# Kernel tuning notes

Hardware: AMD Instinct MI355X
Metric: run time of the kernel (lower is better)

Reference implementation:

```python
import jax, jax.numpy as jnp
import numpy as np

N, E, C, H = 50000, 800000, 64, 64  # nodes, edges, channels, mlp hidden


def _seg_softmax(logits, seg, num_segments):
    # per-destination-node, per-channel softmax over incoming edges (PyG softmax)
    m = jax.ops.segment_max(logits, seg, num_segments=num_segments)
    m = jnp.where(jnp.isfinite(m), m, 0.0)
    e = jnp.exp(logits - m[seg])
    s = jax.ops.segment_sum(e, seg, num_segments=num_segments)
    return e / (s[seg] + 1e-16)


def setup_inputs() -> dict:
    key = jax.random.key(0)
    ks = jax.random.split(key, 16)

    def w(k, shape, fan_in):
        lim = 1.0 / np.sqrt(fan_in)
        return jax.random.uniform(k, shape, jnp.float32, -lim, lim)

    return dict(
        x=jax.random.normal(ks[0], (N, C), jnp.float32),
        pos=jax.random.uniform(ks[1], (N, 3), jnp.float32),
        edge_index=jax.random.randint(ks[2], (2, E), 0, N),
        # lin_in (Linear with bias)
        W_in=w(ks[3], (C, C), C), b_in=jnp.zeros((C,), jnp.float32),
        # PointTransformerConv internal linears (bias=False in PyG)
        W_lin=w(ks[4], (C, C), C),
        W_src=w(ks[5], (C, C), C),
        W_dst=w(ks[6], (C, C), C),
        # pos_nn: Linear(3,64) + ReLU + Linear(64,C)
        Wp1=w(ks[7], (3, H), 3), bp1=jnp.zeros((H,), jnp.float32),
        Wp2=w(ks[8], (H, C), H), bp2=jnp.zeros((C,), jnp.float32),
        # attn_nn: Linear(C,64) + ReLU + Linear(64,C)
        Wa1=w(ks[9], (C, H), C), ba1=jnp.zeros((H,), jnp.float32),
        Wa2=w(ks[10], (H, C), H), ba2=jnp.zeros((C,), jnp.float32),
        # lin_out
        W_out=w(ks[11], (C, C), C), b_out=jnp.zeros((C,), jnp.float32),
    )


def reference(x, pos, edge_index, W_in, b_in, W_lin, W_src, W_dst,
              Wp1, bp1, Wp2, bp2, Wa1, ba1, Wa2, ba2, W_out, b_out):
    n = x.shape[0]
    src, dst = edge_index[0], edge_index[1]
    # lin_in + ReLU
    h = jax.nn.relu(x @ W_in + b_in)                      # [N,C]
    # PointTransformerConv projections
    v = h @ W_lin                                         # values [N,C]
    a_src = h @ W_src                                     # alpha_j source term
    a_dst = h @ W_dst                                     # alpha_i dest term
    # per-edge positional encoding: pos_nn(pos_i - pos_j)
    rel = pos[dst] - pos[src]                             # [E,3]
    delta = jax.nn.relu(rel @ Wp1 + bp1) @ Wp2 + bp2      # [E,C]
    # attention logits: attn_nn(alpha_i - alpha_j + delta)
    alpha = a_dst[dst] - a_src[src] + delta               # [E,C]
    alpha = jax.nn.relu(alpha @ Wa1 + ba1) @ Wa2 + ba2    # [E,C]
    alpha = _seg_softmax(alpha, dst, n)
    # weighted scatter-sum aggregation: sum_j alpha * (x_j + delta)
    out = jax.ops.segment_sum(alpha * (v[src] + delta), dst, num_segments=n)
    # lin_out + ReLU
    return jax.nn.relu(out @ W_out + b_out)
```

## Files before the change

### kernel.cpp

```cpp
#include <hip/hip_runtime.h>

typedef unsigned short u16;
typedef unsigned int   u32;
typedef unsigned long long u64;
typedef __attribute__((ext_vector_type(8))) short bf16x8;
typedef __attribute__((ext_vector_type(4))) float f32x4;

#define DEV static __device__ __forceinline__

DEV u16 f2bf(float f){ union{float f; u32 i;} v; v.f=f; u32 u=v.i;
                       return (u16)((u + 0x7FFFu + ((u>>16)&1u))>>16); }
DEV float bf2f(u16 u){ union{u32 i; float f;} v; v.i=((u32)u)<<16; return v.f; }
DEV float bfl(u32 w){ return bf2f((u16)(w & 0xffffu)); }
DEV float bfh(u32 w){ return bf2f((u16)(w >> 16)); }
DEV u32 pk2(float a, float b){ return (u32)f2bf(a) | ((u32)f2bf(b) << 16); }
DEV void ldsfence(){ asm volatile("s_waitcnt lgkmcnt(0)" ::: "memory"); }
DEV void ldsorder(){ asm volatile("" ::: "memory"); }

#define NBIAS 384
#define FB_P1 0
#define FB_P2 4
#define FB_A1 12
#define FB_A2 20
#define FB_IN 28
#define FB_LIN 36
#define FB_SRC 44
#define FB_DST 52
#define FB_OUT 60
#define NFRAG 68

#define LROW 70
#define LROWD 35

DEV bf16x8 fb_load(const u16* __restrict__ FB, int frag, int lane){
  union{ uint4 u; bf16x8 v; } w;
  w.u = *(const uint4*)(FB + ((size_t)(frag*64+lane))*8);
  return w.v;
}
DEV bf16x8 lds_read_chunk(const u32* l32, int dw){
  union{ u32 d[4]; bf16x8 v; } u;
#pragma unroll
  for(int p=0;p<4;p++) u.d[p] = l32[dw+p];
  return u.v;
}

#define PREP_BLOCKS 19
__global__ __launch_bounds__(256) void k_prep(
  const float* __restrict__ Win, const float* __restrict__ Wlin,
  const float* __restrict__ Wsrc, const float* __restrict__ Wdst,
  const float* __restrict__ Wp1, const float* __restrict__ Wp2,
  const float* __restrict__ Wa1, const float* __restrict__ Wa2,
  const float* __restrict__ Wout,
  const float* __restrict__ bin, const float* __restrict__ bp1, const float* __restrict__ bp2,
  const float* __restrict__ ba1, const float* __restrict__ ba2, const float* __restrict__ bout,
  float* __restrict__ Bf, u16* __restrict__ FB,
  const int* __restrict__ ei, int* __restrict__ deg, int E)
{
  if(blockIdx.x >= PREP_BLOCKS){
    int e = (blockIdx.x - PREP_BLOCKS)*256 + threadIdx.x;
    if(e < E) atomicAdd(&deg[ei[(size_t)E + e]], 1);
    return;
  }
  int idx = blockIdx.x*256 + threadIdx.x;
  if(idx < NBIAS){
    int which = idx >> 6, c = idx & 63;
    if(which == 3){
      float sacc = ba1[c];
      for(int k=0;k<64;k++) sacc += bp2[k]*Wa1[k*64+c];
      Bf[idx] = sacc;
    } else {
      const float* b;
      switch(which){ case 0:b=bin;break; case 1:b=bp1;break; case 2:b=bp2;break;
                     case 4:b=ba2;break; default:b=bout;break; }
      Bf[idx] = b[c];
    }
  } else if(idx < NBIAS + NFRAG*64){
    int j = idx - NBIAS;
    int frag = j >> 6, lane = j & 63;
    int t = lane & 15, q = lane >> 4;
    const float* src = nullptr; const float* fuse = nullptr;
    int K = 64, nt, s;
    if(frag < 4){ src = Wp1; K = 3; nt = frag; s = 0; }
    else if(frag < 12){ int g=frag-4;  src=Wp2;  nt=g>>1; s=g&1; }
    else if(frag < 20){ int g=frag-12; fuse=Wp2; nt=g>>1; s=g&1; }
    else if(frag < 28){ int g=frag-20; src=Wa2;  nt=g>>1; s=g&1; }
    else if(frag < 36){ int g=frag-28; src=Win;  nt=g>>1; s=g&1; }
    else if(frag < 44){ int g=frag-36; src=Wlin; nt=g>>1; s=g&1; }
    else if(frag < 52){ int g=frag-44; fuse=Wsrc; nt=g>>1; s=g&1; }
    else if(frag < 60){ int g=frag-52; fuse=Wdst; nt=g>>1; s=g&1; }
    else              { int g=frag-60; src=Wout; nt=g>>1; s=g&1; }
    u16* dst = FB + ((size_t)(frag*64+lane))*8;
    if(fuse){
      int col = nt*16 + t;
#pragma unroll
      for(int jj=0;jj<8;jj++){
        int k = s*32 + q*8 + jj;
        const float* ar = fuse + k*64;
        float accv = 0.f;
        for(int m=0;m<64;m++) accv += ar[m] * Wa1[m*64+col];
        dst[jj] = f2bf(accv);
      }
    } else {
#pragma unroll
      for(int jj=0;jj<8;jj++){
        int k = s*32 + q*8 + jj;
        dst[jj] = (k<K) ? f2bf(src[k*64 + nt*16 + t]) : (u16)0;
      }
    }
  }
}

__global__ __launch_bounds__(256) void k_scanA(const int* __restrict__ deg,
    int* __restrict__ row_start, int* __restrict__ bsum, int N){
  __shared__ int b[256];
  int tid = threadIdx.x, i = blockIdx.x*256 + tid;
  int v = (i<N) ? deg[i] : 0;
  b[tid] = v; __syncthreads();
#pragma unroll
  for(int off=1; off<256; off<<=1){
    int u = (tid>=off) ? b[tid-off] : 0;
    __syncthreads(); b[tid] += u; __syncthreads();
  }
  if(i<N) row_start[i] = b[tid] - v;
  if(tid==255) bsum[blockIdx.x] = b[255];
}

__global__ __launch_bounds__(256) void k_scanBC(
  const int* __restrict__ bsum, int* __restrict__ row_start, int nb, int N)
{
  __shared__ int b[256];
  __shared__ int ex[256];
  int tid = threadIdx.x;
  int v = (tid<nb) ? bsum[tid] : 0;
  b[tid] = v; __syncthreads();
#pragma unroll
  for(int off=1; off<256; off<<=1){
    int u = (tid>=off) ? b[tid-off] : 0;
    __syncthreads(); b[tid] += u; __syncthreads();
  }
  ex[tid] = b[tid] - v;
  __syncthreads();
  int off0 = ex[blockIdx.x];
  int i = blockIdx.x*256 + tid;
  if(i<N) row_start[i] += off0;
  if(blockIdx.x==0 && tid==255) row_start[N] = b[255];
}

__global__ __launch_bounds__(256) void k_mid2(
  const int* __restrict__ ei, const int* __restrict__ row_start, int* __restrict__ cursor,
  int2* __restrict__ pair, int E, int sblocks,
  const float* __restrict__ x, const float* __restrict__ Bf, const u16* __restrict__ FB,
  u16* __restrict__ vf, u16* __restrict__ asof, u16* __restrict__ adof,
  int N, int ntiles, int nodeblocks,
  float* __restrict__ Z, int zcount4, int zblocks)
{
  __shared__ u16 sc16[4][16*LROW];
  int bid = blockIdx.x;

  if(bid < sblocks){
    int e = bid*256 + threadIdx.x;
    if(e < E){
      int d = ei[(size_t)E + e];
      int p = atomicAdd(&cursor[d], 1);
      int2 pr; pr.x = ei[e]; pr.y = d;
      pair[row_start[d] + p] = pr;
    }
    return;
  }
  if(bid >= sblocks + nodeblocks){
    int zb = bid - sblocks - nodeblocks;
    float4* Z4 = (float4*)Z;
    float4 z = {0.f,0.f,0.f,0.f};
    for(int i = zb*256 + threadIdx.x; i < zcount4; i += zblocks*256) Z4[i] = z;
    return;
  }

  int lane = threadIdx.x & 63, warp = threadIdx.x >> 6;
  int t = lane & 15, q = lane >> 4;
  int tile = (bid - sblocks)*4 + warp;
  if(tile >= ntiles) return;
  u16* lb = sc16[warp]; u32* lb32 = (u32*)lb;
  int r0 = tile*16;
  int row = r0 + t; if(row >= N) row = N-1;

  const float4* x4 = (const float4*)(x + (size_t)row*64);
  bf16x8 xa[2];
#pragma unroll
  for(int s=0;s<2;s++){
    float4 u0 = x4[s*8 + q*2], u1 = x4[s*8 + q*2 + 1];
    xa[s][0]=(short)f2bf(u0.x); xa[s][1]=(short)f2bf(u0.y);
    xa[s][2]=(short)f2bf(u0.z); xa[s][3]=(short)f2bf(u0.w);
    xa[s][4]=(short)f2bf(u1.x); xa[s][5]=(short)f2bf(u1.y);
    xa[s][6]=(short)f2bf(u1.z); xa[s][7]=(short)f2bf(u1.w);
  }
  f32x4 zero = {0.f,0.f,0.f,0.f};
  f32x4 acc[4];
#pragma unroll
  for(int nt=0;nt<4;nt++){
    acc[nt] = __builtin_amdgcn_mfma_f32_16x16x32_bf16(xa[0], fb_load(FB, FB_IN+nt*2+0, lane), zero, 0,0,0);
    acc[nt] = __builtin_amdgcn_mfma_f32_16x16x32_bf16(xa[1], fb_load(FB, FB_IN+nt*2+1, lane), acc[nt], 0,0,0);
  }
#pragma unroll
  for(int nt=0;nt<4;nt++)
#pragma unroll
    for(int r=0;r<4;r++)
      lb[(q*4+r)*LROW + nt*16 + t] = f2bf(fmaxf(acc[nt][r] + Bf[nt*16+t], 0.f));
  ldsfence();
  bf16x8 h0 = lds_read_chunk(lb32, t*LROWD + q*4);
  bf16x8 h1 = lds_read_chunk(lb32, t*LROWD + 16 + q*4);

  const int fb0[3] = {FB_LIN, FB_SRC, FB_DST};
  u16* Os[3] = {vf, asof, adof};
#pragma unroll
  for(int mtx=0; mtx<3; mtx++){
    f32x4 av[4];
#pragma unroll
    for(int nt=0;nt<4;nt++){
      av[nt] = __builtin_amdgcn_mfma_f32_16x16x32_bf16(h0, fb_load(FB, fb0[mtx]+nt*2+0, lane), zero, 0,0,0);
      av[nt] = __builtin_amdgcn_mfma_f32_16x16x32_bf16(h1, fb_load(FB, fb0[mtx]+nt*2+1, lane), av[nt], 0,0,0);
    }
    u16* O = Os[mtx];
#pragma unroll
    for(int r=0;r<4;r++){
      int rr = r0 + q*4 + r;
      if(rr < N){
        uint2 o;
        o.x = (u32)f2bf(av[0][r]) | ((u32)f2bf(av[1][r]) << 16);
        o.y = (u32)f2bf(av[2][r]) | ((u32)f2bf(av[3][r]) << 16);
        *(uint2*)(O + (size_t)rr*64 + t*4) = o;
      }
    }
  }
}

DEV void flushseg(int d, float* numP, float* SP, const int* __restrict__ row_start,
                  float* __restrict__ num, float* __restrict__ S,
                  int lo, int hi, int q, int t){
  if(d < 0) return;
#pragma unroll
  for(int nt=0;nt<4;nt++){
    numP[nt] += __shfl_xor(numP[nt], 16, 64);
    numP[nt] += __shfl_xor(numP[nt], 32, 64);
    SP[nt]   += __shfl_xor(SP[nt],   16, 64);
    SP[nt]   += __shfl_xor(SP[nt],   32, 64);
  }
  bool partial = (row_start[d] < lo) || (row_start[d+1] > hi);
  if(q==0){
#pragma unroll
    for(int nt=0;nt<4;nt++){
      size_t off = (size_t)d*64 + nt*16 + t;
      if(partial){ atomicAdd(&num[off], numP[nt]); atomicAdd(&S[off], SP[nt]); }
      else       { num[off] = numP[nt]; S[off] = SP[nt]; }
    }
  }
#pragma unroll
  for(int nt=0;nt<4;nt++){ numP[nt]=0.f; SP[nt]=0.f; }
}

DEV void agg_tile(int tbase, int hi_w, int lo_w, int did,
                  const float wv[4][4], const float pd[4][4],
                  int& cur_d, float* numP, float* SP,
                  const int* __restrict__ row_start,
                  float* __restrict__ num, float* __restrict__ S, int q, int t){
  int m = 0;
  while(m < 16){
    int d0 = __shfl(did, m, 64);
    u32 same = (u32)(__ballot(did == d0) & 0xFFFFull);
    u32 rest = ~(same >> m);
    int len = __ffs(rest) - 1;
    int m1 = m + len;
    if(d0 != cur_d){
      flushseg(cur_d, numP, SP, row_start, num, S, lo_w, hi_w, q, t);
      cur_d = d0;
    }
#pragma unroll
    for(int r=0;r<4;r++){
      int mm = q*4 + r;
      bool use = (mm >= m) && (mm < m1) && ((tbase+mm) < hi_w);
      if(use){
#pragma unroll
        for(int nt=0;nt<4;nt++){
          numP[nt] += wv[nt][r] * pd[r][nt];
          SP[nt]   += wv[nt][r];
        }
      }
    }
    m = m1;
  }
}

__global__ __launch_bounds__(256,2) void k_edge_p9(
  const int* __restrict__ row_start, const int2* __restrict__ pair,
  const float* __restrict__ pos, const float* __restrict__ Bf, const u16* __restrict__ FB,
  const u16* __restrict__ vf, const u16* __restrict__ asof, const u16* __restrict__ adof,
  float* __restrict__ S, float* __restrict__ num, int E, int nsuper, int spw)
{
  __shared__ u16 sc16[4][2*32*LROW];
  int lane = threadIdx.x & 63, warp = threadIdx.x >> 6;
  int t = lane & 15, q = lane >> 4;
  int wid = blockIdx.x*4 + warp;
  int s0 = wid*spw, s1 = s0 + spw;
  if(s0 >= nsuper) return;
  if(s1 > nsuper) s1 = nsuper;
  int lo = s0*32, hi = s1*32; if(hi > E) hi = E;
  u16* lb = sc16[warp];             u32* lb32 = (u32*)lb;
  u16* lu = sc16[warp] + 32*LROW;   u32* lu32 = (u32*)lu;

  float bp1f[4], bp2f[4], baf[4], ba2f[4];
#pragma unroll
  for(int nt=0;nt<4;nt++){
    bp1f[nt]=Bf[ 64+nt*16+t]; bp2f[nt]=Bf[128+nt*16+t];
    baf[nt] =Bf[192+nt*16+t]; ba2f[nt]=Bf[256+nt*16+t];
  }
  const uint2* ad2 = (const uint2*)adof;
  const uint2* as2 = (const uint2*)asof;
  const uint2* v2  = (const uint2*)vf;
  f32x4 zero = {0.f,0.f,0.f,0.f};
  float numP[4] = {0,0,0,0}, SP[4] = {0,0,0,0};
  int cur_d = -1;

  int2 spA, spB;
  bf16x8 a1A, a1B;
  {
    int ecA = lo + t;      if(ecA >= hi) ecA = hi-1;
    int ecB = lo + 16 + t; if(ecB >= hi) ecB = hi-1;
    spA = pair[ecA]; spB = pair[ecB];
#pragma unroll
    for(int j=0;j<8;j++){ a1A[j]=0; a1B[j]=0; }
    if(q==0){
      a1A[0] = (short)f2bf(pos[(size_t)spA.y*3+0] - pos[(size_t)spA.x*3+0]);
      a1A[1] = (short)f2bf(pos[(size_t)spA.y*3+1] - pos[(size_t)spA.x*3+1]);
      a1A[2] = (short)f2bf(pos[(size_t)spA.y*3+2] - pos[(size_t)spA.x*3+2]);
      a1B[0] = (short)f2bf(pos[(size_t)spB.y*3+0] - pos[(size_t)spB.x*3+0]);
      a1B[1] = (short)f2bf(pos[(size_t)spB.y*3+1] - pos[(size_t)spB.x*3+1]);
      a1B[2] = (short)f2bf(pos[(size_t)spB.y*3+2] - pos[(size_t)spB.x*3+2]);
    }
  }

  for(int tb = lo; tb < hi; tb += 32){
    bool hasB = (tb+16) < hi;
    int didA = spA.y, didB = spB.y;

    int2 nspA, nspB;
    {
      int eA = tb + 32 + t; if(eA >= hi) eA = hi-1;
      int eB = tb + 48 + t; if(eB >= hi) eB = hi-1;
      nspA = pair[eA]; nspB = pair[eB];
    }
    uint2 adwA[4], aswA[4];
#pragma unroll
    for(int r=0;r<4;r++){
      int e = tb + q*4 + r; if(e >= hi) e = hi-1;
      int2 p = pair[e];
      adwA[r] = ad2[(size_t)p.y*16 + t];
      aswA[r] = as2[(size_t)p.x*16 + t];
    }
    uint2 adwB[4], aswB[4];
#pragma unroll
    for(int r=0;r<4;r++){
      int e = tb + 16 + q*4 + r; if(e >= hi) e = hi-1;
      int2 p = pair[e];
      adwB[r] = ad2[(size_t)p.y*16 + t];
      aswB[r] = as2[(size_t)p.x*16 + t];
    }
    uint2 vrawA[4], vrawB[4];
#pragma unroll
    for(int r=0;r<4;r++){
      int e = tb + q*4 + r; if(e >= hi) e = hi-1;
      vrawA[r] = v2[(size_t)pair[e].x*16 + t];
    }
#pragma unroll
    for(int r=0;r<4;r++){
      int e = tb + 16 + q*4 + r; if(e >= hi) e = hi-1;
      vrawB[r] = v2[(size_t)pair[e].x*16 + t];
    }

    f32x4 accA[4], accB[4];
#pragma unroll
    for(int nt=0;nt<4;nt++){
      bf16x8 wp = fb_load(FB, FB_P1+nt, lane);
      accA[nt] = __builtin_amdgcn_mfma_f32_16x16x32_bf16(a1A, wp, zero, 0,0,0);
      accB[nt] = __builtin_amdgcn_mfma_f32_16x16x32_bf16(a1B, wp, zero, 0,0,0);
    }

#pragma unroll
    for(int nt=0;nt<4;nt++)
#pragma unroll
      for(int r=0;r<4;r++){
        lb[(     q*4+r)*LROW + nt*16 + t] = f2bf(fmaxf(accA[nt][r] + bp1f[nt], 0.f));
        lb[(16 + q*4+r)*LROW + nt*16 + t] = f2bf(fmaxf(accB[nt][r] + bp1f[nt], 0.f));
      }
    ldsorder();

    bf16x8 atA0 = lds_read_chunk(lb32, (t   )*LROWD + q*4);
    bf16x8 atA1 = lds_read_chunk(lb32, (t   )*LROWD + 16 + q*4);
    bf16x8 atB0 = lds_read_chunk(lb32, (t+16)*LROWD + q*4);
    bf16x8 atB1 = lds_read_chunk(lb32, (t+16)*LROWD + 16 + q*4);

    bf16x8 na1A, na1B;
#pragma unroll
    for(int j=0;j<8;j++){ na1A[j]=0; na1B[j]=0; }
    if(q==0){
      na1A[0] = (short)f2bf(pos[(size_t)nspA.y*3+0] - pos[(size_t)nspA.x*3+0]);
      na1A[1] = (short)f2bf(pos[(size_t)nspA.y*3+1] - pos[(size_t)nspA.x*3+1]);
      na1A[2] = (short)f2bf(pos[(size_t)nspA.y*3+2] - pos[(size_t)nspA.x*3+2]);
      na1B[0] = (short)f2bf(pos[(size_t)nspB.y*3+0] - pos[(size_t)nspB.x*3+0]);
      na1B[1] = (short)f2bf(pos[(size_t)nspB.y*3+1] - pos[(size_t)nspB.x*3+1]);
      na1B[2] = (short)f2bf(pos[(size_t)nspB.y*3+2] - pos[(size_t)nspB.x*3+2]);
    }

    u32 dpA[4][2], dpB[4][2];
#pragma unroll
    for(int nt=0;nt<4;nt++){
      bf16x8 w0 = fb_load(FB, FB_P2+nt*2+0, lane);
      bf16x8 w1 = fb_load(FB, FB_P2+nt*2+1, lane);
      f32x4 a = __builtin_amdgcn_mfma_f32_16x16x32_bf16(atA0, w0, zero, 0,0,0);
      a = __builtin_amdgcn_mfma_f32_16x16x32_bf16(atA1, w1, a, 0,0,0);
      f32x4 b = __builtin_amdgcn_mfma_f32_16x16x32_bf16(atB0, w0, zero, 0,0,0);
      b = __builtin_amdgcn_mfma_f32_16x16x32_bf16(atB1, w1, b, 0,0,0);
      dpA[nt][0] = pk2(a[0]+bp2f[nt], a[1]+bp2f[nt]);
      dpA[nt][1] = pk2(a[2]+bp2f[nt], a[3]+bp2f[nt]);
      dpB[nt][0] = pk2(b[0]+bp2f[nt], b[1]+bp2f[nt]);
      dpB[nt][1] = pk2(b[2]+bp2f[nt], b[3]+bp2f[nt]);
    }

#pragma unroll
    for(int nt=0;nt<4;nt++){
      bf16x8 w0 = fb_load(FB, FB_A1+nt*2+0, lane);
      bf16x8 w1 = fb_load(FB, FB_A1+nt*2+1, lane);
      f32x4 a = __builtin_amdgcn_mfma_f32_16x16x32_bf16(atA0, w0, zero, 0,0,0);
      a = __builtin_amdgcn_mfma_f32_16x16x32_bf16(atA1, w1, a, 0,0,0);
#pragma unroll
      for(int r=0;r<4;r++){
        u32 dw = (nt&2)? adwA[r].y : adwA[r].x;
        u32 sw = (nt&2)? aswA[r].y : aswA[r].x;
        float c = ((nt&1)? bfh(dw) : bfl(dw)) - ((nt&1)? bfh(sw) : bfl(sw));
        lu[(q*4+r)*LROW + nt*16 + t] = f2bf(fmaxf(a[r] + c + baf[nt], 0.f));
      }
    }
#pragma unroll
    for(int nt=0;nt<4;nt++){
      bf16x8 w0 = fb_load(FB, FB_A1+nt*2+0, lane);
      bf16x8 w1 = fb_load(FB, FB_A1+nt*2+1, lane);
      f32x4 b = __builtin_amdgcn_mfma_f32_16x16x32_bf16(atB0, w0, zero, 0,0,0);
      b = __builtin_amdgcn_mfma_f32_16x16x32_bf16(atB1, w1, b, 0,0,0);
#pragma unroll
      for(int r=0;r<4;r++){
        u32 dw = (nt&2)? adwB[r].y : adwB[r].x;
        u32 sw = (nt&2)? aswB[r].y : aswB[r].x;
        float c = ((nt&1)? bfh(dw) : bfl(dw)) - ((nt&1)? bfh(sw) : bfl(sw));
        lu[(16 + q*4+r)*LROW + nt*16 + t] = f2bf(fmaxf(b[r] + c + baf[nt], 0.f));
      }
    }
    ldsorder();

    bf16x8 auA0 = lds_read_chunk(lu32, (t   )*LROWD + q*4);
    bf16x8 auA1 = lds_read_chunk(lu32, (t   )*LROWD + 16 + q*4);
    bf16x8 auB0 = lds_read_chunk(lu32, (t+16)*LROWD + q*4);
    bf16x8 auB1 = lds_read_chunk(lu32, (t+16)*LROWD + 16 + q*4);

    float wv[4][4], pd[4][4];
#pragma unroll
    for(int nt=0;nt<4;nt++){
      bf16x8 w0 = fb_load(FB, FB_A2+nt*2+0, lane);
      bf16x8 w1 = fb_load(FB, FB_A2+nt*2+1, lane);
      f32x4 a = __builtin_amdgcn_mfma_f32_16x16x32_bf16(auA0, w0, zero, 0,0,0);
      a = __builtin_amdgcn_mfma_f32_16x16x32_bf16(auA1, w1, a, 0,0,0);
#pragma unroll
      for(int r=0;r<4;r++)
        wv[nt][r] = ((tb + q*4 + r) < hi) ? __expf(fminf(a[r] + ba2f[nt], 80.f)) : 0.f;
    }
#pragma unroll
    for(int r=0;r<4;r++){
      float va[4] = { bfl(vrawA[r].x), bfh(vrawA[r].x), bfl(vrawA[r].y), bfh(vrawA[r].y) };
#pragma unroll
      for(int nt=0;nt<4;nt++){
        u32 dw = dpA[nt][r>>1];
        pd[r][nt] = va[nt] + ((r&1)? bfh(dw) : bfl(dw));
      }
    }
    agg_tile(tb, hi, lo, didA, wv, pd, cur_d, numP, SP, row_start, num, S, q, t);

    if(hasB){
#pragma unroll
      for(int nt=0;nt<4;nt++){
        bf16x8 w0 = fb_load(FB, FB_A2+nt*2+0, lane);
        bf16x8 w1 = fb_load(FB, FB_A2+nt*2+1, lane);
        f32x4 b = __builtin_amdgcn_mfma_f32_16x16x32_bf16(auB0, w0, zero, 0,0,0);
        b = __builtin_amdgcn_mfma_f32_16x16x32_bf16(auB1, w1, b, 0,0,0);
#pragma unroll
        for(int r=0;r<4;r++)
          wv[nt][r] = ((tb + 16 + q*4 + r) < hi) ? __expf(fminf(b[r] + ba2f[nt], 80.f)) : 0.f;
      }
#pragma unroll
      for(int r=0;r<4;r++){
        float vb[4] = { bfl(vrawB[r].x), bfh(vrawB[r].x), bfl(vrawB[r].y), bfh(vrawB[r].y) };
#pragma unroll
        for(int nt=0;nt<4;nt++){
          u32 dw = dpB[nt][r>>1];
          pd[r][nt] = vb[nt] + ((r&1)? bfh(dw) : bfl(dw));
        }
      }
      agg_tile(tb+16, hi, lo, didB, wv, pd, cur_d, numP, SP, row_start, num, S, q, t);
    }

    spA = nspA; spB = nspB; a1A = na1A; a1B = na1B;
  }
  flushseg(cur_d, numP, SP, row_start, num, S, lo, hi, q, t);
}

__global__ __launch_bounds__(256) void k_out_m(
  const float* __restrict__ num, const float* __restrict__ S,
  const float* __restrict__ Bf, const u16* __restrict__ FB,
  float* __restrict__ out, int N, int ntiles)
{
  int lane = threadIdx.x & 63, warp = threadIdx.x >> 6;
  int t = lane & 15, q = lane >> 4;
  int tile = blockIdx.x*4 + warp;
  if(tile >= ntiles) return;
  int r0 = tile*16;
  int row = r0 + t; if(row >= N) row = N-1;
  const float4* n4 = (const float4*)(num + (size_t)row*64);
  const float4* s4 = (const float4*)(S   + (size_t)row*64);
  bf16x8 af[2];
#pragma unroll
  for(int s=0;s<2;s++){
    float4 n0 = n4[s*8 + q*2], n1 = n4[s*8 + q*2 + 1];
    float4 s0 = s4[s*8 + q*2], s1 = s4[s*8 + q*2 + 1];
    af[s][0]=(short)f2bf(n0.x/(s0.x+1e-16f)); af[s][1]=(short)f2bf(n0.y/(s0.y+1e-16f));
    af[s][2]=(short)f2bf(n0.z/(s0.z+1e-16f)); af[s][3]=(short)f2bf(n0.w/(s0.w+1e-16f));
    af[s][4]=(short)f2bf(n1.x/(s1.x+1e-16f)); af[s][5]=(short)f2bf(n1.y/(s1.y+1e-16f));
    af[s][6]=(short)f2bf(n1.z/(s1.z+1e-16f)); af[s][7]=(short)f2bf(n1.w/(s1.w+1e-16f));
  }
  f32x4 zero = {0.f,0.f,0.f,0.f};
#pragma unroll
  for(int nt=0;nt<4;nt++){
    f32x4 a = __builtin_amdgcn_mfma_f32_16x16x32_bf16(af[0], fb_load(FB, FB_OUT+nt*2+0, lane), zero, 0,0,0);
    a = __builtin_amdgcn_mfma_f32_16x16x32_bf16(af[1], fb_load(FB, FB_OUT+nt*2+1, lane), a, 0,0,0);
    float b = Bf[320 + nt*16 + t];
#pragma unroll
    for(int r=0;r<4;r++){
      int rr = r0 + q*4 + r;
      if(rr < N) out[(size_t)rr*64 + nt*16 + t] = fmaxf(a[r] + b, 0.f);
    }
  }
}

extern "C" void kernel_launch(void* const* d_in, const int* in_sizes, int n_in,
                              void* d_out, int out_size, void* d_ws, size_t ws_size,
                              hipStream_t stream){
  const float* x   =(const float*)d_in[0];
  const float* pos =(const float*)d_in[1];
  const int*   ei  =(const int*)d_in[2];
  const float* Win =(const float*)d_in[3];  const float* bin=(const float*)d_in[4];
  const float* Wlin=(const float*)d_in[5];  const float* Wsrc=(const float*)d_in[6];
  const float* Wdst=(const float*)d_in[7];
  const float* Wp1 =(const float*)d_in[8];  const float* bp1=(const float*)d_in[9];
  const float* Wp2 =(const float*)d_in[10]; const float* bp2=(const float*)d_in[11];
  const float* Wa1 =(const float*)d_in[12]; const float* ba1=(const float*)d_in[13];
  const float* Wa2 =(const float*)d_in[14]; const float* ba2=(const float*)d_in[15];
  const float* Wout=(const float*)d_in[16]; const float* bout=(const float*)d_in[17];
  int N = in_sizes[0]/64;
  int E = in_sizes[2]/2;

  float* Bf    = (float*)d_ws;
  u16*   FB    = (u16*)(Bf + NBIAS);
  u16*   vfb   = FB + (size_t)NFRAG*64*8;
  u16*   asb   = vfb + (size_t)N*64;
  u16*   adb   = asb + (size_t)N*64;
  float* S     = (float*)(adb + (size_t)N*64);
  float* num   = S    + (size_t)N*64;
  int* deg       = (int*)(num + (size_t)N*64);
  int* cursor    = deg + N;
  int* row_start = cursor + N;
  int* bsum      = row_start + (N+1);
  int* bsoff     = bsum + 256;
  int2* pair     = (int2*)(bsoff + 256);

  int ntiles = (N+15)/16;
  int nsuper = (E+31)/32;
  int total_waves = 2048;
  int spw = (nsuper + total_waves - 1) / total_waves;
  int nwaves = (nsuper + spw - 1) / spw;
  int eblocks = (nwaves + 3) / 4;
  int nscb = (N+255)/256;
  int hblocks = (E+255)/256;
  int nodeblocks = (ntiles+3)/4;
  int sblocks = (E+255)/256;
  int zblocks = 512;
  int zcount4 = N*32;

  hipMemsetAsync(deg, 0, (size_t)2*N*sizeof(int), stream);
  k_prep<<<dim3(PREP_BLOCKS + hblocks), dim3(256), 0, stream>>>(
      Win,Wlin,Wsrc,Wdst,Wp1,Wp2,Wa1,Wa2,Wout,
      bin,bp1,bp2,ba1,ba2,bout, Bf, FB, ei, deg, E);
  k_scanA<<<dim3(nscb), dim3(256), 0, stream>>>(deg, row_start, bsum, N);
  k_scanBC<<<dim3(nscb), dim3(256), 0, stream>>>(bsum, row_start, nscb, N);
  k_mid2<<<dim3(sblocks + nodeblocks + zblocks), dim3(256), 0, stream>>>(
      ei, row_start, cursor, pair, E, sblocks,
      x, Bf, FB, vfb, asb, adb, N, ntiles, nodeblocks,
      S, zcount4, zblocks);
  k_edge_p9<<<dim3(eblocks), dim3(256), 0, stream>>>(row_start, pair, pos, Bf, FB,
                                                     vfb, asb, adb, S, num, E, nsuper, spw);
  k_out_m<<<dim3((ntiles+3)/4), dim3(256), 0, stream>>>(num, S, Bf, FB, (float*)d_out, N, ntiles);
}
```

Baseline: 331.5 us.

## Process three 16-edge sub-tiles per edge-kernel iteration and defer value gathers

The edge kernel now handles 48 edges per loop iteration (three 16-row MFMA sub-tiles A/B/C) instead of 32. The per-warp LDS scratch and the super-tile size grow to match. The value-vector gathers move later, after the attention first-layer MFMAs, so their latency can overlap with compute. The aim is more independent gathers and MFMAs in flight per iteration, at the cost of more registers and LDS, which may cut occupancy under launch_bounds(256,2) or cause spills.

```diff
diff --git a/kernel.cpp b/kernel.cpp
--- a/kernel.cpp
+++ b/kernel.cpp
@@ -289,22 +289,22 @@
   }
 }
 
-__global__ __launch_bounds__(256,2) void k_edge_p9(
+__global__ __launch_bounds__(256,2) void k_edge_p10(
   const int* __restrict__ row_start, const int2* __restrict__ pair,
   const float* __restrict__ pos, const float* __restrict__ Bf, const u16* __restrict__ FB,
   const u16* __restrict__ vf, const u16* __restrict__ asof, const u16* __restrict__ adof,
   float* __restrict__ S, float* __restrict__ num, int E, int nsuper, int spw)
 {
-  __shared__ u16 sc16[4][2*32*LROW];
+  __shared__ u16 sc16[4][2*48*LROW];
   int lane = threadIdx.x & 63, warp = threadIdx.x >> 6;
   int t = lane & 15, q = lane >> 4;
   int wid = blockIdx.x*4 + warp;
   int s0 = wid*spw, s1 = s0 + spw;
   if(s0 >= nsuper) return;
   if(s1 > nsuper) s1 = nsuper;
-  int lo = s0*32, hi = s1*32; if(hi > E) hi = E;
+  int lo = s0*48, hi = s1*48; if(hi > E) hi = E;
   u16* lb = sc16[warp];             u32* lb32 = (u32*)lb;
-  u16* lu = sc16[warp] + 32*LROW;   u32* lu32 = (u32*)lu;
+  u16* lu = sc16[warp] + 48*LROW;   u32* lu32 = (u32*)lu;
 
   float bp1f[4], bp2f[4], baf[4], ba2f[4];
 #pragma unroll
@@ -319,14 +319,15 @@
   float numP[4] = {0,0,0,0}, SP[4] = {0,0,0,0};
   int cur_d = -1;
 
-  int2 spA, spB;
-  bf16x8 a1A, a1B;
+  int2 spA, spB, spC;
+  bf16x8 a1A, a1B, a1C;
   {
     int ecA = lo + t;      if(ecA >= hi) ecA = hi-1;
     int ecB = lo + 16 + t; if(ecB >= hi) ecB = hi-1;
-    spA = pair[ecA]; spB = pair[ecB];
-#pragma unroll
-    for(int j=0;j<8;j++){ a1A[j]=0; a1B[j]=0; }
+    int ecC = lo + 32 + t; if(ecC >= hi) ecC = hi-1;
+    spA = pair[ecA]; spB = pair[ecB]; spC = pair[ecC];
+#pragma unroll
+    for(int j=0;j<8;j++){ a1A[j]=0; a1B[j]=0; a1C[j]=0; }
     if(q==0){
       a1A[0] = (short)f2bf(pos[(size_t)spA.y*3+0] - pos[(size_t)spA.x*3+0]);
       a1A[1] = (short)f2bf(pos[(size_t)spA.y*3+1] - pos[(size_t)spA.x*3+1]);
@@ -334,18 +335,22 @@
       a1B[0] = (short)f2bf(pos[(size_t)spB.y*3+0] - pos[(size_t)spB.x*3+0]);
       a1B[1] = (short)f2bf(pos[(size_t)spB.y*3+1] - pos[(size_t)spB.x*3+1]);
       a1B[2] = (short)f2bf(pos[(size_t)spB.y*3+2] - pos[(size_t)spB.x*3+2]);
-    }
-  }
-
-  for(int tb = lo; tb < hi; tb += 32){
-    bool hasB = (tb+16) < hi;
-    int didA = spA.y, didB = spB.y;
-
-    int2 nspA, nspB;
+      a1C[0] = (short)f2bf(pos[(size_t)spC.y*3+0] - pos[(size_t)spC.x*3+0]);
+      a1C[1] = (short)f2bf(pos[(size_t)spC.y*3+1] - pos[(size_t)spC.x*3+1]);
+      a1C[2] = (short)f2bf(pos[(size_t)spC.y*3+2] - pos[(size_t)spC.x*3+2]);
+    }
+  }
+
+  for(int tb = lo; tb < hi; tb += 48){
+    bool hasB = (tb+16) < hi, hasC = (tb+32) < hi;
+    int didA = spA.y, didB = spB.y, didC = spC.y;
+
+    int2 nspA, nspB, nspC;
     {
-      int eA = tb + 32 + t; if(eA >= hi) eA = hi-1;
-      int eB = tb + 48 + t; if(eB >= hi) eB = hi-1;
-      nspA = pair[eA]; nspB = pair[eB];
+      int eA = tb + 48 + t; if(eA >= hi) eA = hi-1;
+      int eB = tb + 64 + t; if(eB >= hi) eB = hi-1;
+      int eC = tb + 80 + t; if(eC >= hi) eC = hi-1;
+      nspA = pair[eA]; nspB = pair[eB]; nspC = pair[eC];
     }
     uint2 adwA[4], aswA[4];
 #pragma unroll
@@ -363,24 +368,14 @@
       adwB[r] = ad2[(size_t)p.y*16 + t];
       aswB[r] = as2[(size_t)p.x*16 + t];
     }
-    uint2 vrawA[4], vrawB[4];
-#pragma unroll
-    for(int r=0;r<4;r++){
-      int e = tb + q*4 + r; if(e >= hi) e = hi-1;
-      vrawA[r] = v2[(size_t)pair[e].x*16 + t];
-    }
-#pragma unroll
-    for(int r=0;r<4;r++){
-      int e = tb + 16 + q*4 + r; if(e >= hi) e = hi-1;
-      vrawB[r] = v2[(size_t)pair[e].x*16 + t];
-    }
-
-    f32x4 accA[4], accB[4];
+
+    f32x4 accA[4], accB[4], accC[4];
 #pragma unroll
     for(int nt=0;nt<4;nt++){
       bf16x8 wp = fb_load(FB, FB_P1+nt, lane);
       accA[nt] = __builtin_amdgcn_mfma_f32_16x16x32_bf16(a1A, wp, zero, 0,0,0);
       accB[nt] = __builtin_amdgcn_mfma_f32_16x16x32_bf16(a1B, wp, zero, 0,0,0);
+      accC[nt] = __builtin_amdgcn_mfma_f32_16x16x32_bf16(a1C, wp, zero, 0,0,0);
     }
 
 #pragma unroll
@@ -389,6 +384,7 @@
       for(int r=0;r<4;r++){
         lb[(     q*4+r)*LROW + nt*16 + t] = f2bf(fmaxf(accA[nt][r] + bp1f[nt], 0.f));
         lb[(16 + q*4+r)*LROW + nt*16 + t] = f2bf(fmaxf(accB[nt][r] + bp1f[nt], 0.f));
+        lb[(32 + q*4+r)*LROW + nt*16 + t] = f2bf(fmaxf(accC[nt][r] + bp1f[nt], 0.f));
       }
     ldsorder();
 
@@ -396,10 +392,12 @@
     bf16x8 atA1 = lds_read_chunk(lb32, (t   )*LROWD + 16 + q*4);
     bf16x8 atB0 = lds_read_chunk(lb32, (t+16)*LROWD + q*4);
     bf16x8 atB1 = lds_read_chunk(lb32, (t+16)*LROWD + 16 + q*4);
-
-    bf16x8 na1A, na1B;
-#pragma unroll
-    for(int j=0;j<8;j++){ na1A[j]=0; na1B[j]=0; }
+    bf16x8 atC0 = lds_read_chunk(lb32, (t+32)*LROWD + q*4);
+    bf16x8 atC1 = lds_read_chunk(lb32, (t+32)*LROWD + 16 + q*4);
+
+    bf16x8 na1A, na1B, na1C;
+#pragma unroll
+    for(int j=0;j<8;j++){ na1A[j]=0; na1B[j]=0; na1C[j]=0; }
     if(q==0){
       na1A[0] = (short)f2bf(pos[(size_t)nspA.y*3+0] - pos[(size_t)nspA.x*3+0]);
       na1A[1] = (short)f2bf(pos[(size_t)nspA.y*3+1] - pos[(size_t)nspA.x*3+1]);
@@ -407,9 +405,12 @@
       na1B[0] = (short)f2bf(pos[(size_t)nspB.y*3+0] - pos[(size_t)nspB.x*3+0]);
       na1B[1] = (short)f2bf(pos[(size_t)nspB.y*3+1] - pos[(size_t)nspB.x*3+1]);
       na1B[2] = (short)f2bf(pos[(size_t)nspB.y*3+2] - pos[(size_t)nspB.x*3+2]);
-    }
-
-    u32 dpA[4][2], dpB[4][2];
+      na1C[0] = (short)f2bf(pos[(size_t)nspC.y*3+0] - pos[(size_t)nspC.x*3+0]);
+      na1C[1] = (short)f2bf(pos[(size_t)nspC.y*3+1] - pos[(size_t)nspC.x*3+1]);
+      na1C[2] = (short)f2bf(pos[(size_t)nspC.y*3+2] - pos[(size_t)nspC.x*3+2]);
+    }
+
+    u32 dpA[4][2], dpB[4][2], dpC[4][2];
 #pragma unroll
     for(int nt=0;nt<4;nt++){
       bf16x8 w0 = fb_load(FB, FB_P2+nt*2+0, lane);
@@ -418,18 +419,20 @@
       a = __builtin_amdgcn_mfma_f32_16x16x32_bf16(atA1, w1, a, 0,0,0);
       f32x4 b = __builtin_amdgcn_mfma_f32_16x16x32_bf16(atB0, w0, zero, 0,0,0);
       b = __builtin_amdgcn_mfma_f32_16x16x32_bf16(atB1, w1, b, 0,0,0);
+      f32x4 c = __builtin_amdgcn_mfma_f32_16x16x32_bf16(atC0, w0, zero, 0,0,0);
+      c = __builtin_amdgcn_mfma_f32_16x16x32_bf16(atC1, w1, c, 0,0,0);
       dpA[nt][0] = pk2(a[0]+bp2f[nt], a[1]+bp2f[nt]);
       dpA[nt][1] = pk2(a[2]+bp2f[nt], a[3]+bp2f[nt]);
       dpB[nt][0] = pk2(b[0]+bp2f[nt], b[1]+bp2f[nt]);
       dpB[nt][1] = pk2(b[2]+bp2f[nt], b[3]+bp2f[nt]);
-    }
-
-#pragma unroll
-    for(int nt=0;nt<4;nt++){
-      bf16x8 w0 = fb_load(FB, FB_A1+nt*2+0, lane);
-      bf16x8 w1 = fb_load(FB, FB_A1+nt*2+1, lane);
-      f32x4 a = __builtin_amdgcn_mfma_f32_16x16x32_bf16(atA0, w0, zero, 0,0,0);
-      a = __builtin_amdgcn_mfma_f32_16x16x32_bf16(atA1, w1, a, 0,0,0);
+      dpC[nt][0] = pk2(c[0]+bp2f[nt], c[1]+bp2f[nt]);
+      dpC[nt][1] = pk2(c[2]+bp2f[nt], c[3]+bp2f[nt]);
+    }
+
+#pragma unroll
+    for(int nt=0;nt<4;nt++){
+      f32x4 a = __builtin_amdgcn_mfma_f32_16x16x32_bf16(atA0, fb_load(FB, FB_A1+nt*2+0, lane), zero, 0,0,0);
+      a = __builtin_amdgcn_mfma_f32_16x16x32_bf16(atA1, fb_load(FB, FB_A1+nt*2+1, lane), a, 0,0,0);
 #pragma unroll
       for(int r=0;r<4;r++){
         u32 dw = (nt&2)? adwA[r].y : adwA[r].x;
@@ -438,12 +441,20 @@
         lu[(q*4+r)*LROW + nt*16 + t] = f2bf(fmaxf(a[r] + c + baf[nt], 0.f));
       }
     }
-#pragma unroll
-    for(int nt=0;nt<4;nt++){
-      bf16x8 w0 = fb_load(FB, FB_A1+nt*2+0, lane);
-      bf16x8 w1 = fb_load(FB, FB_A1+nt*2+1, lane);
-      f32x4 b = __builtin_amdgcn_mfma_f32_16x16x32_bf16(atB0, w0, zero, 0,0,0);
-      b = __builtin_amdgcn_mfma_f32_16x16x32_bf16(atB1, w1, b, 0,0,0);
+
+    uint2 adwC[4], aswC[4];
+#pragma unroll
+    for(int r=0;r<4;r++){
+      int e = tb + 32 + q*4 + r; if(e >= hi) e = hi-1;
+      int2 p = pair[e];
+      adwC[r] = ad2[(size_t)p.y*16 + t];
+      aswC[r] = as2[(size_t)p.x*16 + t];
+    }
+
+#pragma unroll
+    for(int nt=0;nt<4;nt++){
+      f32x4 b = __builtin_amdgcn_mfma_f32_16x16x32_bf16(atB0, fb_load(FB, FB_A1+nt*2+0, lane), zero, 0,0,0);
+      b = __builtin_amdgcn_mfma_f32_16x16x32_bf16(atB1, fb_load(FB, FB_A1+nt*2+1, lane), b, 0,0,0);
 #pragma unroll
       for(int r=0;r<4;r++){
         u32 dw = (nt&2)? adwB[r].y : adwB[r].x;
@@ -452,12 +463,43 @@
         lu[(16 + q*4+r)*LROW + nt*16 + t] = f2bf(fmaxf(b[r] + c + baf[nt], 0.f));
       }
     }
+#pragma unroll
+    for(int nt=0;nt<4;nt++){
+      f32x4 c4 = __builtin_amdgcn_mfma_f32_16x16x32_bf16(atC0, fb_load(FB, FB_A1+nt*2+0, lane), zero, 0,0,0);
+      c4 = __builtin_amdgcn_mfma_f32_16x16x32_bf16(atC1, fb_load(FB, FB_A1+nt*2+1, lane), c4, 0,0,0);
+#pragma unroll
+      for(int r=0;r<4;r++){
+        u32 dw = (nt&2)? adwC[r].y : adwC[r].x;
+        u32 sw = (nt&2)? aswC[r].y : aswC[r].x;
+        float c = ((nt&1)? bfh(dw) : bfl(dw)) - ((nt&1)? bfh(sw) : bfl(sw));
+        lu[(32 + q*4+r)*LROW + nt*16 + t] = f2bf(fmaxf(c4[r] + c + baf[nt], 0.f));
+      }
+    }
+
+    uint2 vrawA[4], vrawB[4], vrawC[4];
+#pragma unroll
+    for(int r=0;r<4;r++){
+      int e = tb + q*4 + r; if(e >= hi) e = hi-1;
+      vrawA[r] = v2[(size_t)pair[e].x*16 + t];
+    }
+#pragma unroll
+    for(int r=0;r<4;r++){
+      int e = tb + 16 + q*4 + r; if(e >= hi) e = hi-1;
+      vrawB[r] = v2[(size_t)pair[e].x*16 + t];
+    }
+#pragma unroll
+    for(int r=0;r<4;r++){
+      int e = tb + 32 + q*4 + r; if(e >= hi) e = hi-1;
+      vrawC[r] = v2[(size_t)pair[e].x*16 + t];
+    }
     ldsorder();
 
     bf16x8 auA0 = lds_read_chunk(lu32, (t   )*LROWD + q*4);
     bf16x8 auA1 = lds_read_chunk(lu32, (t   )*LROWD + 16 + q*4);
     bf16x8 auB0 = lds_read_chunk(lu32, (t+16)*LROWD + q*4);
     bf16x8 auB1 = lds_read_chunk(lu32, (t+16)*LROWD + 16 + q*4);
+    bf16x8 auC0 = lds_read_chunk(lu32, (t+32)*LROWD + q*4);
+    bf16x8 auC1 = lds_read_chunk(lu32, (t+32)*LROWD + 16 + q*4);
 
     float wv[4][4], pd[4][4];
 #pragma unroll
@@ -504,7 +546,31 @@
       agg_tile(tb+16, hi, lo, didB, wv, pd, cur_d, numP, SP, row_start, num, S, q, t);
     }
 
-    spA = nspA; spB = nspB; a1A = na1A; a1B = na1B;
+    if(hasC){
+#pragma unroll
+      for(int nt=0;nt<4;nt++){
+        bf16x8 w0 = fb_load(FB, FB_A2+nt*2+0, lane);
+        bf16x8 w1 = fb_load(FB, FB_A2+nt*2+1, lane);
+        f32x4 c4 = __builtin_amdgcn_mfma_f32_16x16x32_bf16(auC0, w0, zero, 0,0,0);
+        c4 = __builtin_amdgcn_mfma_f32_16x16x32_bf16(auC1, w1, c4, 0,0,0);
+#pragma unroll
+        for(int r=0;r<4;r++)
+          wv[nt][r] = ((tb + 32 + q*4 + r) < hi) ? __expf(fminf(c4[r] + ba2f[nt], 80.f)) : 0.f;
+      }
+#pragma unroll
+      for(int r=0;r<4;r++){
+        float vc[4] = { bfl(vrawC[r].x), bfh(vrawC[r].x), bfl(vrawC[r].y), bfh(vrawC[r].y) };
+#pragma unroll
+        for(int nt=0;nt<4;nt++){
+          u32 dw = dpC[nt][r>>1];
+          pd[r][nt] = vc[nt] + ((r&1)? bfh(dw) : bfl(dw));
+        }
+      }
+      agg_tile(tb+32, hi, lo, didC, wv, pd, cur_d, numP, SP, row_start, num, S, q, t);
+    }
+
+    spA = nspA; spB = nspB; spC = nspC;
+    a1A = na1A; a1B = na1B; a1C = na1C;
   }
   flushseg(cur_d, numP, SP, row_start, num, S, lo, hi, q, t);
 }
@@ -578,7 +644,7 @@
   int2* pair     = (int2*)(bsoff + 256);
 
   int ntiles = (N+15)/16;
-  int nsuper = (E+31)/32;
+  int nsuper = (E+47)/48;
   int total_waves = 2048;
   int spw = (nsuper + total_waves - 1) / total_waves;
   int nwaves = (nsuper + spw - 1) / spw;
@@ -600,7 +666,7 @@
       ei, row_start, cursor, pair, E, sblocks,
       x, Bf, FB, vfb, asb, adb, N, ntiles, nodeblocks,
       S, zcount4, zblocks);
-  k_edge_p9<<<dim3(eblocks), dim3(256), 0, stream>>>(row_start, pair, pos, Bf, FB,
-                                                     vfb, asb, adb, S, num, E, nsuper, spw);
+  k_edge_p10<<<dim3(eblocks), dim3(256), 0, stream>>>(row_start, pair, pos, Bf, FB,
+                                                      vfb, asb, adb, S, num, E, nsuper, spw);
   k_out_m<<<dim3((ntiles+3)/4), dim3(256), 0, stream>>>(num, S, Bf, FB, (float*)d_out, N, ntiles);
 }
```

New measurement: 419.5 us. 1.27x slower.
